# Kernel tuning notes

Hardware: AMD Instinct MI355X
Metric: run time of the kernel (lower is better)

## Reference

```python
import jax, jax.numpy as jnp
import numpy as np

V, D, H, C = 100000, 300, 16, 5
B, T = 256, 128


def setup_inputs() -> dict:
    key = jax.random.key(0)
    ks = jax.random.split(key, 8)
    s = 1.0 / np.sqrt(H).astype(np.float32)  # PyTorch LSTM/Linear init range
    x = jax.random.randint(ks[0], (B, T), 0, V)
    emb = jax.random.normal(ks[1], (V, D), jnp.float32) * 0.02
    W_ih = jax.random.uniform(ks[2], (4 * H, D), jnp.float32, -s, s)
    W_hh = jax.random.uniform(ks[3], (4 * H, H), jnp.float32, -s, s)
    b_ih = jax.random.uniform(ks[4], (4 * H,), jnp.float32, -s, s)
    b_hh = jax.random.uniform(ks[5], (4 * H,), jnp.float32, -s, s)
    W_out = jax.random.uniform(ks[6], (C, H), jnp.float32, -s, s)
    b_out = jax.random.uniform(ks[7], (C,), jnp.float32, -s, s)
    return dict(x=x, emb=emb, W_ih=W_ih, W_hh=W_hh, b_ih=b_ih, b_hh=b_hh,
                W_out=W_out, b_out=b_out)


def reference(x, emb, W_ih, W_hh, b_ih, b_hh, W_out, b_out):
    h_dim = W_hh.shape[1]
    xe = emb[x]  # [B,T,D] embedding lookup
    # Precompute input contribution to all 4 gates for all timesteps (one big GEMM).
    xg = jnp.einsum('btd,gd->btg', xe, W_ih) + b_ih + b_hh  # [B,T,4H]
    xg = jnp.transpose(xg, (1, 0, 2))  # [T,B,4H] time-major for scan
    b = x.shape[0]
    h0 = jnp.zeros((b, h_dim), xg.dtype)
    c0 = jnp.zeros((b, h_dim), xg.dtype)

    def step(carry, g_t):
        h, c = carry
        g = g_t + h @ W_hh.T  # [B,4H]
        i, f, gg, o = jnp.split(g, 4, axis=-1)  # PyTorch gate order: i,f,g,o
        i = jax.nn.sigmoid(i)
        f = jax.nn.sigmoid(f)
        gg = jnp.tanh(gg)
        o = jax.nn.sigmoid(o)
        c = f * c + i * gg
        h = o * jnp.tanh(c)
        return (h, c), h

    _, hs = jax.lax.scan(step, (h0, c0), xg)  # hs: [T,B,H]
    hs = jnp.transpose(hs, (1, 0, 2))  # [B,T,H]
    return hs @ W_out.T + b_out  # [B,T,C]
```

## Files before the change

kernel.cpp:

```cpp
#include <hip/hip_runtime.h>
#include <hip/hip_bf16.h>
#include <cstdint>

#define BB   256
#define TT   128
#define DD   300
#define HH   16
#define GG   64
#define CC   5
#define ROWS (BB*TT)

__global__ __launch_bounds__(256) void xg_gemm_kernel(
    const int* __restrict__ x, const float* __restrict__ emb,
    const float* __restrict__ W_ih, const float* __restrict__ b_ih,
    const float* __restrict__ b_hh, float* __restrict__ xg) {

  __shared__ float As[64][60];
  __shared__ float Ws[60][68];
  __shared__ int   xidx[64];

  const int t  = threadIdx.x;
  const int tx = t & 15;
  const int ty = t >> 4;
  const int row0 = blockIdx.x * 64;

  if (t < 64) xidx[t] = x[row0 + t];

  float acc[4][4] = {};

  for (int ch = 0; ch < 5; ch++) {
    const int dbase = ch * 60;
    __syncthreads();

    for (int u = t; u < 960; u += 256) {
      int r = u / 15, f = u - r * 15;
      const float* src = emb + (size_t)xidx[r] * DD + dbase + f * 4;
      *(float4*)&As[r][f * 4] = *(const float4*)src;
    }
    for (int u = t; u < 960; u += 256) {
      int c = u / 15, f = u - c * 15;
      float4 w = *(const float4*)&W_ih[c * DD + dbase + f * 4];
      Ws[f * 4 + 0][c] = w.x;
      Ws[f * 4 + 1][c] = w.y;
      Ws[f * 4 + 2][c] = w.z;
      Ws[f * 4 + 3][c] = w.w;
    }
    __syncthreads();

#pragma unroll
    for (int q = 0; q < 15; q++) {
      float4 wq[4];
      wq[0] = *(const float4*)&Ws[q * 4 + 0][tx * 4];
      wq[1] = *(const float4*)&Ws[q * 4 + 1][tx * 4];
      wq[2] = *(const float4*)&Ws[q * 4 + 2][tx * 4];
      wq[3] = *(const float4*)&Ws[q * 4 + 3][tx * 4];
      const float* wf = (const float*)wq;
#pragma unroll
      for (int r = 0; r < 4; r++) {
        float4 a = *(const float4*)&As[ty * 4 + r][q * 4];
#pragma unroll
        for (int c = 0; c < 4; c++) {
          acc[r][c] = fmaf(a.x, wf[0 * 4 + c], acc[r][c]);
          acc[r][c] = fmaf(a.y, wf[1 * 4 + c], acc[r][c]);
          acc[r][c] = fmaf(a.z, wf[2 * 4 + c], acc[r][c]);
          acc[r][c] = fmaf(a.w, wf[3 * 4 + c], acc[r][c]);
        }
      }
    }
  }

  float bias[4];
#pragma unroll
  for (int c = 0; c < 4; c++)
    bias[c] = b_ih[tx * 4 + c] + b_hh[tx * 4 + c];

#pragma unroll
  for (int r = 0; r < 4; r++) {
    float4 o;
    o.x = acc[r][0] + bias[0];
    o.y = acc[r][1] + bias[1];
    o.z = acc[r][2] + bias[2];
    o.w = acc[r][3] + bias[3];
    *(float4*)&xg[(size_t)(row0 + ty * 4 + r) * GG + tx * 4] = o;
  }
}

__global__ __launch_bounds__(256) void lstm_seq_kernel(
    const float* __restrict__ xg, const float* __restrict__ W_hh,
    const float* __restrict__ W_out, const float* __restrict__ b_out,
    float* __restrict__ out) {

  __shared__ float xgs[TT * GG];
  __shared__ float hs[TT][HH];

  const int t = threadIdx.x;
  const int b = blockIdx.x;

  {
    const float4* __restrict__ src = (const float4*)(xg + (size_t)b * TT * GG);
    float4* dst = (float4*)xgs;
#pragma unroll
    for (int i = 0; i < 32; i++) {
      int idx = i * 256 + t;
      dst[idx] = src[idx];
    }
  }
  __syncthreads();

  if (t < 64) {
    const int lane = t;
    const int k = lane & 15;
    const int gate = lane >> 4;
    const float gscale = (gate == 2) ? -2.0f : -1.0f;
    const bool is_tanh = (gate == 2);

    float wh[16];
    {
      const float* wr = W_hh + lane * HH;
#pragma unroll
      for (int kk = 0; kk < 16; kk++) wh[kk] = wr[kk];
    }

    float c = 0.0f;
    float hu[16];
#pragma unroll
    for (int kk = 0; kk < 16; kk++) hu[kk] = 0.0f;

    float g = xgs[lane];
    for (int tstep = 0; tstep < TT; tstep++) {
      float gnext = xgs[((tstep + 1) & 127) * GG + lane];

      float a0 = fmaf(hu[0], wh[0], g);
      a0 = fmaf(hu[1], wh[1], a0);
      a0 = fmaf(hu[2], wh[2], a0);
      a0 = fmaf(hu[3], wh[3], a0);
      float a1 = hu[4] * wh[4];
      a1 = fmaf(hu[5], wh[5], a1);
      a1 = fmaf(hu[6], wh[6], a1);
      a1 = fmaf(hu[7], wh[7], a1);
      float a2 = hu[8] * wh[8];
      a2 = fmaf(hu[9], wh[9], a2);
      a2 = fmaf(hu[10], wh[10], a2);
      a2 = fmaf(hu[11], wh[11], a2);
      float a3 = hu[12] * wh[12];
      a3 = fmaf(hu[13], wh[13], a3);
      a3 = fmaf(hu[14], wh[14], a3);
      a3 = fmaf(hu[15], wh[15], a3);
      float gv_ = (a0 + a1) + (a2 + a3);

      float e = __expf(gv_ * gscale);
      float s = __builtin_amdgcn_rcpf(1.0f + e);
      float act = is_tanh ? (2.0f * s - 1.0f) : s;

      float iv = __shfl(act, k);
      float fv = __shfl(act, k + 16);
      float gg = __shfl(act, k + 32);
      float ov = __shfl(act, k + 48);

      c = fmaf(fv, c, iv * gg);
      float e2 = __expf(-2.0f * c);
      float tc = fmaf(2.0f, __builtin_amdgcn_rcpf(1.0f + e2), -1.0f);
      float hnew = ov * tc;

      if (lane < 16) hs[tstep][lane] = hnew;

#pragma unroll
      for (int kk = 0; kk < 16; kk++)
        hu[kk] = __uint_as_float(__builtin_amdgcn_readlane(__float_as_uint(hnew), kk));

      g = gnext;
    }
  }
  __syncthreads();

  float* outb = out + (size_t)b * TT * CC;
  for (int idx = t; idx < TT * CC; idx += 256) {
    int tt = idx / CC;
    int cc = idx - tt * CC;
    const float* wr = W_out + cc * HH;
    float accv = b_out[cc];
#pragma unroll
    for (int kk = 0; kk < 16; kk++) accv = fmaf(hs[tt][kk], wr[kk], accv);
    outb[idx] = accv;
  }
}

extern "C" void kernel_launch(void* const* d_in, const int* in_sizes, int n_in,
                              void* d_out, int out_size, void* d_ws, size_t ws_size,
                              hipStream_t stream) {
  const int*   x     = (const int*)d_in[0];
  const float* emb   = (const float*)d_in[1];
  const float* W_ih  = (const float*)d_in[2];
  const float* W_hh  = (const float*)d_in[3];
  const float* b_ih  = (const float*)d_in[4];
  const float* b_hh  = (const float*)d_in[5];
  const float* W_out = (const float*)d_in[6];
  const float* b_out = (const float*)d_in[7];
  float* out = (float*)d_out;
  float* xg  = (float*)d_ws;

  xg_gemm_kernel<<<ROWS / 64, 256, 0, stream>>>(x, emb, W_ih, b_ih, b_hh, xg);
  lstm_seq_kernel<<<BB, 256, 0, stream>>>(xg, W_hh, W_out, b_out, out);
}
```

Before: 223.3 us.

## Fuse input-projection GEMM into per-batch LSTM kernel with register prefetch

Merges the embedding-gather GEMM and the sequential LSTM into one kernel per batch row, so the xg gate pre-activations stay in shared memory and never go through global memory. Each block now computes all 128 timesteps' GEMM (8 rows per thread) and software-prefetches the next K-chunk into registers while computing the current one. It also switches the exp calls to exp2f with a log2(e) scale. The risks are that the GEMM phase now runs on only 256 blocks, with more registers and more LDS per block, which may lower occupancy.

After: 236.5 us. 1.06x slower.

```diff
diff --git a/kernel.cpp b/kernel.cpp
--- a/kernel.cpp
+++ b/kernel.cpp
@@ -1,69 +1,108 @@
 #include <hip/hip_runtime.h>
-#include <hip/hip_bf16.h>
 #include <cstdint>
 
-#define BB   256
-#define TT   128
-#define DD   300
-#define HH   16
-#define GG   64
-#define CC   5
-#define ROWS (BB*TT)
-
-__global__ __launch_bounds__(256) void xg_gemm_kernel(
+#define BB 256
+#define TT 128
+#define DD 300
+#define HH 16
+#define GG 64
+#define CC 5
+#define KC 60
+#define NCH 5
+
+__global__ __launch_bounds__(256) void lstm_fused_kernel(
     const int* __restrict__ x, const float* __restrict__ emb,
-    const float* __restrict__ W_ih, const float* __restrict__ b_ih,
-    const float* __restrict__ b_hh, float* __restrict__ xg) {
-
-  __shared__ float As[64][60];
-  __shared__ float Ws[60][68];
-  __shared__ int   xidx[64];
+    const float* __restrict__ W_ih, const float* __restrict__ W_hh,
+    const float* __restrict__ b_ih, const float* __restrict__ b_hh,
+    const float* __restrict__ W_out, const float* __restrict__ b_out,
+    float* __restrict__ out) {
+
+  __shared__ float As[TT * KC];
+  __shared__ float Ws[KC * 68];
+  __shared__ float xgs[TT * GG];
+  __shared__ float hsm[TT * HH];
+  __shared__ int   xid[TT];
 
   const int t  = threadIdx.x;
+  const int b  = blockIdx.x;
   const int tx = t & 15;
   const int ty = t >> 4;
-  const int row0 = blockIdx.x * 64;
-
-  if (t < 64) xidx[t] = x[row0 + t];
-
-  float acc[4][4] = {};
-
-  for (int ch = 0; ch < 5; ch++) {
-    const int dbase = ch * 60;
+
+  if (t < TT) xid[t] = x[b * TT + t];
+  __syncthreads();
+
+  const int na = (t < 128) ? 8 : 7;
+  const int nw = (t < 192) ? 4 : 3;
+
+  float4 apf[8];
+  float4 wpf[4];
+
+  auto load_chunk = [&](int dbase) {
+#pragma unroll
+    for (int i = 0; i < 8; i++) {
+      if (i < na) {
+        int u = t + 256 * i;
+        int r = u / 15, f = u - r * 15;
+        apf[i] = *(const float4*)(emb + (size_t)xid[r] * DD + dbase + 4 * f);
+      }
+    }
+#pragma unroll
+    for (int i = 0; i < 4; i++) {
+      if (i < nw) {
+        int u = t + 256 * i;
+        int c = u / 15, f = u - c * 15;
+        wpf[i] = *(const float4*)(W_ih + c * DD + dbase + 4 * f);
+      }
+    }
+  };
+
+  auto store_chunk = [&]() {
+#pragma unroll
+    for (int i = 0; i < 8; i++) {
+      if (i < na) {
+        int u = t + 256 * i;
+        int r = u / 15, f = u - r * 15;
+        *(float4*)&As[r * KC + 4 * f] = apf[i];
+      }
+    }
+#pragma unroll
+    for (int i = 0; i < 4; i++) {
+      if (i < nw) {
+        int u = t + 256 * i;
+        int c = u / 15, f = u - c * 15;
+        Ws[(4 * f + 0) * 68 + c] = wpf[i].x;
+        Ws[(4 * f + 1) * 68 + c] = wpf[i].y;
+        Ws[(4 * f + 2) * 68 + c] = wpf[i].z;
+        Ws[(4 * f + 3) * 68 + c] = wpf[i].w;
+      }
+    }
+  };
+
+  float acc[8][4] = {};
+
+  load_chunk(0);
+  for (int ch = 0; ch < NCH; ch++) {
+    if (ch > 0) __syncthreads();
+    store_chunk();
     __syncthreads();
-
-    for (int u = t; u < 960; u += 256) {
-      int r = u / 15, f = u - r * 15;
-      const float* src = emb + (size_t)xidx[r] * DD + dbase + f * 4;
-      *(float4*)&As[r][f * 4] = *(const float4*)src;
-    }
-    for (int u = t; u < 960; u += 256) {
-      int c = u / 15, f = u - c * 15;
-      float4 w = *(const float4*)&W_ih[c * DD + dbase + f * 4];
-      Ws[f * 4 + 0][c] = w.x;
-      Ws[f * 4 + 1][c] = w.y;
-      Ws[f * 4 + 2][c] = w.z;
-      Ws[f * 4 + 3][c] = w.w;
-    }
-    __syncthreads();
+    if (ch + 1 < NCH) load_chunk((ch + 1) * KC);
 
 #pragma unroll
     for (int q = 0; q < 15; q++) {
-      float4 wq[4];
-      wq[0] = *(const float4*)&Ws[q * 4 + 0][tx * 4];
-      wq[1] = *(const float4*)&Ws[q * 4 + 1][tx * 4];
-      wq[2] = *(const float4*)&Ws[q * 4 + 2][tx * 4];
-      wq[3] = *(const float4*)&Ws[q * 4 + 3][tx * 4];
-      const float* wf = (const float*)wq;
-#pragma unroll
-      for (int r = 0; r < 4; r++) {
-        float4 a = *(const float4*)&As[ty * 4 + r][q * 4];
+      float4 wc[4];
+#pragma unroll
+      for (int j = 0; j < 4; j++)
+        wc[j] = *(const float4*)&Ws[(q * 4 + j) * 68 + tx * 4];
+#pragma unroll
+      for (int r = 0; r < 8; r++) {
+        const int row = ty + 16 * r;
+        float4 a = *(const float4*)&As[row * KC + q * 4];
 #pragma unroll
         for (int c = 0; c < 4; c++) {
-          acc[r][c] = fmaf(a.x, wf[0 * 4 + c], acc[r][c]);
-          acc[r][c] = fmaf(a.y, wf[1 * 4 + c], acc[r][c]);
-          acc[r][c] = fmaf(a.z, wf[2 * 4 + c], acc[r][c]);
-          acc[r][c] = fmaf(a.w, wf[3 * 4 + c], acc[r][c]);
+          acc[r][c] = fmaf(a.x, ((const float*)&wc[0])[c], acc[r][c]);
+          acc[r][c] = fmaf(a.y, ((const float*)&wc[1])[c], acc[r][c]);
+          acc[r][c] = fmaf(a.z, ((const float*)&wc[2])[c], acc[r][c]);
+          acc[r][c] = fmaf(a.w, ((const float*)&wc[3])[c], acc[r][c]);
         }
       }
     }
@@ -73,37 +112,15 @@
 #pragma unroll
   for (int c = 0; c < 4; c++)
     bias[c] = b_ih[tx * 4 + c] + b_hh[tx * 4 + c];
-
-#pragma unroll
-  for (int r = 0; r < 4; r++) {
+#pragma unroll
+  for (int r = 0; r < 8; r++) {
+    const int row = ty + 16 * r;
     float4 o;
     o.x = acc[r][0] + bias[0];
     o.y = acc[r][1] + bias[1];
     o.z = acc[r][2] + bias[2];
     o.w = acc[r][3] + bias[3];
-    *(float4*)&xg[(size_t)(row0 + ty * 4 + r) * GG + tx * 4] = o;
-  }
-}
-
-__global__ __launch_bounds__(256) void lstm_seq_kernel(
-    const float* __restrict__ xg, const float* __restrict__ W_hh,
-    const float* __restrict__ W_out, const float* __restrict__ b_out,
-    float* __restrict__ out) {
-
-  __shared__ float xgs[TT * GG];
-  __shared__ float hs[TT][HH];
-
-  const int t = threadIdx.x;
-  const int b = blockIdx.x;
-
-  {
-    const float4* __restrict__ src = (const float4*)(xg + (size_t)b * TT * GG);
-    float4* dst = (float4*)xgs;
-#pragma unroll
-    for (int i = 0; i < 32; i++) {
-      int idx = i * 256 + t;
-      dst[idx] = src[idx];
-    }
+    *(float4*)&xgs[row * GG + tx * 4] = o;
   }
   __syncthreads();
 
@@ -111,8 +128,9 @@
     const int lane = t;
     const int k = lane & 15;
     const int gate = lane >> 4;
-    const float gscale = (gate == 2) ? -2.0f : -1.0f;
     const bool is_tanh = (gate == 2);
+    const float L2E = 1.4426950408889634f;
+    const float gscale = is_tanh ? (-2.0f * L2E) : (-L2E);
 
     float wh[16];
     {
@@ -148,7 +166,7 @@
       a3 = fmaf(hu[15], wh[15], a3);
       float gv_ = (a0 + a1) + (a2 + a3);
 
-      float e = __expf(gv_ * gscale);
+      float e = exp2f(gv_ * gscale);
       float s = __builtin_amdgcn_rcpf(1.0f + e);
       float act = is_tanh ? (2.0f * s - 1.0f) : s;
 
@@ -158,11 +176,11 @@
       float ov = __shfl(act, k + 48);
 
       c = fmaf(fv, c, iv * gg);
-      float e2 = __expf(-2.0f * c);
+      float e2 = exp2f(-2.0f * L2E * c);
       float tc = fmaf(2.0f, __builtin_amdgcn_rcpf(1.0f + e2), -1.0f);
       float hnew = ov * tc;
 
-      if (lane < 16) hs[tstep][lane] = hnew;
+      if (lane < 16) hsm[tstep * HH + lane] = hnew;
 
 #pragma unroll
       for (int kk = 0; kk < 16; kk++)
@@ -180,7 +198,7 @@
     const float* wr = W_out + cc * HH;
     float accv = b_out[cc];
 #pragma unroll
-    for (int kk = 0; kk < 16; kk++) accv = fmaf(hs[tt][kk], wr[kk], accv);
+    for (int kk = 0; kk < 16; kk++) accv = fmaf(hsm[tt * HH + kk], wr[kk], accv);
     outb[idx] = accv;
   }
 }
@@ -197,8 +215,7 @@
   const float* W_out = (const float*)d_in[6];
   const float* b_out = (const float*)d_in[7];
   float* out = (float*)d_out;
-  float* xg  = (float*)d_ws;
-
-  xg_gemm_kernel<<<ROWS / 64, 256, 0, stream>>>(x, emb, W_ih, b_ih, b_hh, xg);
-  lstm_seq_kernel<<<BB, 256, 0, stream>>>(xg, W_hh, W_out, b_out, out);
+
+  lstm_fused_kernel<<<BB, 256, 0, stream>>>(x, emb, W_ih, W_hh, b_ih, b_hh,
+                                            W_out, b_out, out);
 }
```
